# Performance work log

Measured on AMD Instinct MI355X. Metric: run time of the kernel, lower is better.

Reference implementation:

```python
import jax, jax.numpy as jnp
import numpy as np

N = 50000          # nodes
E_EDGES = 800000   # edges (before self loops)
IN_F = 256
HEADS = 4
OUT_F = 64
NEG_SLOPE = 0.2    # PyG GATv2Conv default negative_slope
EPS_GN = 1e-5      # GraphNorm eps


def setup_inputs() -> dict:
    key = jax.random.key(0)
    ks = jax.random.split(key, 8)
    X = jax.random.normal(ks[0], (N, IN_F), jnp.float32)
    E = jax.random.randint(ks[1], (2, E_EDGES), 0, N, jnp.int32)
    s_in = 1.0 / np.sqrt(IN_F)
    Wl = jax.random.normal(ks[2], (IN_F, HEADS * OUT_F), jnp.float32) * s_in   # lin_l (source)
    Wr = jax.random.normal(ks[3], (IN_F, HEADS * OUT_F), jnp.float32) * s_in   # lin_r (target)
    att = jax.random.normal(ks[4], (HEADS, OUT_F), jnp.float32) / np.sqrt(OUT_F)
    bias = jnp.zeros((OUT_F,), jnp.float32)           # concat=False -> bias of size out_channels
    gn_weight = jnp.ones((OUT_F,), jnp.float32)       # GraphNorm gamma
    gn_bias = jnp.zeros((OUT_F,), jnp.float32)        # GraphNorm beta
    gn_mean_scale = jnp.ones((OUT_F,), jnp.float32)   # GraphNorm alpha
    return {"X": X, "E": E, "Wl": Wl, "Wr": Wr, "att": att, "bias": bias,
            "gn_weight": gn_weight, "gn_bias": gn_bias, "gn_mean_scale": gn_mean_scale}


def reference(X, E, Wl, Wr, att, bias, gn_weight, gn_bias, gn_mean_scale):
    # --- GATv2Conv (heads=HEADS, concat=False, add_self_loops=True, eval: no dropout) ---
    loop = jnp.arange(N, dtype=E.dtype)
    src = jnp.concatenate([E[0], loop])   # [Et]
    dst = jnp.concatenate([E[1], loop])   # [Et]
    xl = (X @ Wl).reshape(N, HEADS, OUT_F)  # source transform
    xr = (X @ Wr).reshape(N, HEADS, OUT_F)  # target transform
    # per-edge attention logits: a^T LeakyReLU(xl_j + xr_i)
    e = jax.nn.leaky_relu(xl[src] + xr[dst], NEG_SLOPE)        # [Et, H, C]
    logits = jnp.einsum('ehc,hc->eh', e, att)                  # [Et, H]
    # segment softmax over incoming edges of each destination node
    m = jax.lax.stop_gradient(jax.ops.segment_max(logits, dst, num_segments=N))
    p = jnp.exp(logits - m[dst])
    denom = jax.ops.segment_sum(p, dst, num_segments=N)
    alpha = p / (denom[dst] + 1e-16)                           # [Et, H]
    out = jax.ops.segment_sum(xl[src] * alpha[:, :, None], dst, num_segments=N)  # [N, H, C]
    out = out.mean(axis=1) + bias                              # concat=False -> mean over heads
    # --- GraphNorm (single graph) ---
    mu = out.mean(axis=0)
    xc = out - gn_mean_scale * mu
    var = (xc * xc).mean(axis=0)
    return gn_weight * xc * jax.lax.rsqrt(var + EPS_GN) + gn_bias
```

## Files before the change

kernel.cpp:

```cpp
#include <hip/hip_runtime.h>
#include <hip/hip_bf16.h>

#define IN_F   256
#define HEADS  4
#define OUT_F  64
#define HF     (HEADS * OUT_F)
#define NOUT   512
#define MAXDEG 128

typedef __bf16 bf16x8 __attribute__((ext_vector_type(8)));
typedef float  f32x4  __attribute__((ext_vector_type(4)));
typedef float  f32x2  __attribute__((ext_vector_type(2)));

__device__ __forceinline__ unsigned short f2bf(float f) {
    unsigned u = __float_as_uint(f);
    return (unsigned short)((u + 0x7FFFu + ((u >> 16) & 1u)) >> 16);
}
__device__ __forceinline__ void gld_lds16(const unsigned short* g, unsigned short* lds_base) {
    __builtin_amdgcn_global_load_lds(
        (const __attribute__((address_space(1))) unsigned int*)g,
        (__attribute__((address_space(3))) unsigned int*)lds_base,
        16, 0, 0);
}
__device__ __forceinline__ f32x2 up2(int u) {
    f32x2 r;
    r.x = __uint_as_float(((unsigned)u) << 16);
    r.y = __uint_as_float(((unsigned)u) & 0xFFFF0000u);
    return r;
}
__device__ __forceinline__ f32x2 max2(f32x2 a, f32x2 b) {
    f32x2 r; r.x = fmaxf(a.x, b.x); r.y = fmaxf(a.y, b.y); return r;
}

__global__ __launch_bounds__(256) void prep(
    const float* __restrict__ X, const float* __restrict__ Wl,
    const float* __restrict__ Wr,
    unsigned short* __restrict__ Xb, unsigned short* __restrict__ Wt,
    int* __restrict__ zero32, int M, int Mp, int Z)
{
    const int b = blockIdx.x, t = threadIdx.x;
    const int idx = b * 256 + t;

    if (idx < Mp * 64) {
        int e = idx * 4;
        int row = e >> 8;
        float4 v = make_float4(0.f, 0.f, 0.f, 0.f);
        if (row < M) v = *(const float4*)(X + e);
        ushort4 o;
        o.x = f2bf(v.x); o.y = f2bf(v.y); o.z = f2bf(v.z); o.w = f2bf(v.w);
        *(ushort4*)(Xb + e) = o;
    }
    if (b < NOUT) {
        const float* W = (b < HF) ? Wl : Wr;
        Wt[b * IN_F + t] = f2bf(W[t * HF + (b & (HF - 1))]);
    }
    if (b >= NOUT) {
        int zi = (b - NOUT) * 256 + t;
        if (zi < Z) zero32[zi] = 0;
    }
}

__global__ __launch_bounds__(256, 2) void gemm_scatter(
    const unsigned short* __restrict__ Xb,
    const unsigned short* __restrict__ Wt,
    unsigned short* __restrict__ xlr,
    const int* __restrict__ E, int* __restrict__ deg,
    int* __restrict__ ssrc, int EE, int SB)
{
    __shared__ __align__(16) unsigned short As[128 * 64];
    __shared__ __align__(16) unsigned short Bs[256 * 64];

    if (blockIdx.x < SB) {
        int i = (blockIdx.x * 256 + threadIdx.x) * 4;
        if (i >= EE) return;
        int4 s4 = *(const int4*)(E + i);
        int4 d4 = *(const int4*)(E + EE + i);
        int p0 = atomicAdd(&deg[d4.x], 1);
        int p1 = atomicAdd(&deg[d4.y], 1);
        int p2 = atomicAdd(&deg[d4.z], 1);
        int p3 = atomicAdd(&deg[d4.w], 1);
        if (p0 < MAXDEG) ssrc[d4.x * MAXDEG + p0] = s4.x;
        if (p1 < MAXDEG) ssrc[d4.y * MAXDEG + p1] = s4.y;
        if (p2 < MAXDEG) ssrc[d4.z * MAXDEG + p2] = s4.z;
        if (p3 < MAXDEG) ssrc[d4.w * MAXDEG + p3] = s4.w;
        return;
    }

    const int g    = blockIdx.x - SB;
    const int tid  = threadIdx.x;
    const int w    = tid >> 6;
    const int lane = tid & 63;
    const int m0   = (g >> 1) * 128;
    const int n0   = (g & 1) * 256;
    const int wm   = (w >> 1) * 64;
    const int wn   = (w & 1) * 128;

    f32x4 acc[4][8];
    #pragma unroll
    for (int i = 0; i < 4; ++i)
        #pragma unroll
        for (int j = 0; j < 8; ++j)
            #pragma unroll
            for (int r = 0; r < 4; ++r) acc[i][j][r] = 0.f;

    const int lr = lane >> 3;
    const int ls = lane & 7;

    for (int k0 = 0; k0 < IN_F; k0 += 64) {
        #pragma unroll
        for (int i = 0; i < 4; ++i) {
            int r = w * 32 + i * 8 + lr;
            int c = ls ^ (r & 7);
            gld_lds16(Xb + (size_t)(m0 + r) * IN_F + k0 + c * 8, &As[(w * 32 + i * 8) * 64]);
        }
        #pragma unroll
        for (int i = 0; i < 8; ++i) {
            int r = w * 64 + i * 8 + lr;
            int c = ls ^ (r & 7);
            gld_lds16(Wt + (size_t)(n0 + r) * IN_F + k0 + c * 8, &Bs[(w * 64 + i * 8) * 64]);
        }
        __syncthreads();

        #pragma unroll
        for (int t = 0; t < 2; ++t) {
            bf16x8 af[4], bfr[8];
            #pragma unroll
            for (int i = 0; i < 4; ++i) {
                int m = wm + i * 16 + (lane & 15);
                int s = (t * 4 + (lane >> 4)) ^ (lane & 7);
                af[i] = __builtin_bit_cast(bf16x8, *(const int4*)&As[m * 64 + s * 8]);
            }
            #pragma unroll
            for (int j = 0; j < 8; ++j) {
                int n = wn + j * 16 + (lane & 15);
                int s = (t * 4 + (lane >> 4)) ^ (lane & 7);
                bfr[j] = __builtin_bit_cast(bf16x8, *(const int4*)&Bs[n * 64 + s * 8]);
            }
            #pragma unroll
            for (int i = 0; i < 4; ++i)
                #pragma unroll
                for (int j = 0; j < 8; ++j)
                    acc[i][j] = __builtin_amdgcn_mfma_f32_16x16x32_bf16(
                        af[i], bfr[j], acc[i][j], 0, 0, 0);
        }
        __syncthreads();
    }

    #pragma unroll
    for (int j = 0; j < 8; ++j) {
        int gc = n0 + wn + j * 16 + (lane & 15);
        #pragma unroll
        for (int i = 0; i < 4; ++i) {
            int gr0 = m0 + wm + i * 16 + (lane >> 4) * 4;
            #pragma unroll
            for (int r = 0; r < 4; ++r)
                xlr[(size_t)(gr0 + r) * NOUT + gc] = f2bf(acc[i][j][r]);
        }
    }
}

__global__ __launch_bounds__(128) void aggr_csr(
    const unsigned short* __restrict__ xlr, const float* __restrict__ att,
    const int* __restrict__ deg, const int* __restrict__ ssrc,
    float* __restrict__ accum, int N)
{
    const int v = blockIdx.x * 2 + (threadIdx.x >> 6);
    if (v >= N) return;
    const int lane = threadIdx.x & 63;
    const int hw = lane >> 5;
    const int h  = (lane >> 3) & 3;
    const int q  = lane & 7;
    const int cbase = h * OUT_F + q * 8;

    const float L2E = 1.44269504088896f;
    f32x2 at2[4];
    {
        float4 a0 = *(const float4*)(att + cbase);
        float4 a1 = *(const float4*)(att + cbase + 4);
        at2[0].x = L2E * a0.x; at2[0].y = L2E * a0.y;
        at2[1].x = L2E * a0.z; at2[1].y = L2E * a0.w;
        at2[2].x = L2E * a1.x; at2[2].y = L2E * a1.y;
        at2[3].x = L2E * a1.z; at2[3].y = L2E * a1.w;
    }
    f32x2 r2[4];
    {
        int4 ru = *(const int4*)(xlr + (size_t)v * NOUT + HF + cbase);
        r2[0] = up2(ru.x); r2[1] = up2(ru.y); r2[2] = up2(ru.z); r2[3] = up2(ru.w);
    }

    f32x2 S0 = {0.f,0.f}, S1 = {0.f,0.f}, S2 = {0.f,0.f}, S3 = {0.f,0.f};
    float den = 0.f;

    const int o0 = v * MAXDEG;
    const int items = deg[v] + 1;
    const unsigned short* xbase = xlr + cbase;

    for (int e0 = 0; e0 < items; e0 += 64) {
        int it = e0 + lane;
        int sv = v;
        if (it > 0 && it < items) sv = ssrc[o0 + it - 1];
        const int nch = min(64, items - e0);
        const int npair = (nch + 1) >> 1;

        int j = 0;
        for (; j + 2 <= npair; j += 2) {
            const int iA = 2 * j + hw, iB = iA + 2;
            const int sA = __shfl(sv, iA, 64);
            const int sB = __shfl(sv, iB, 64);
            int4 uA = *(const int4*)(xbase + (size_t)sA * NOUT);
            int4 uB = *(const int4*)(xbase + (size_t)sB * NOUT);
            f32x2 a0 = up2(uA.x), a1 = up2(uA.y), a2 = up2(uA.z), a3 = up2(uA.w);
            f32x2 b0 = up2(uB.x), b1 = up2(uB.y), b2 = up2(uB.z), b3 = up2(uB.w);
            f32x2 sa0 = a0 + r2[0], sa1 = a1 + r2[1], sa2 = a2 + r2[2], sa3 = a3 + r2[3];
            f32x2 sb0 = b0 + r2[0], sb1 = b1 + r2[1], sb2 = b2 + r2[2], sb3 = b3 + r2[3];
            f32x2 tA2 = max2(sa0, 0.2f * sa0) * at2[0];
            tA2 += max2(sa1, 0.2f * sa1) * at2[1];
            tA2 += max2(sa2, 0.2f * sa2) * at2[2];
            tA2 += max2(sa3, 0.2f * sa3) * at2[3];
            f32x2 tB2 = max2(sb0, 0.2f * sb0) * at2[0];
            tB2 += max2(sb1, 0.2f * sb1) * at2[1];
            tB2 += max2(sb2, 0.2f * sb2) * at2[2];
            tB2 += max2(sb3, 0.2f * sb3) * at2[3];
            float tA = tA2.x + tA2.y, tB = tB2.x + tB2.y;
            tA += __shfl_xor(tA, 1, 64); tB += __shfl_xor(tB, 1, 64);
            tA += __shfl_xor(tA, 2, 64); tB += __shfl_xor(tB, 2, 64);
            tA += __shfl_xor(tA, 4, 64); tB += __shfl_xor(tB, 4, 64);
            float pA = ((e0 + iA) < items) ? exp2f(tA) : 0.f;
            float pB = ((e0 + iB) < items) ? exp2f(tB) : 0.f;
            den += pA + pB;
            S0 += pA * a0 + pB * b0;
            S1 += pA * a1 + pB * b1;
            S2 += pA * a2 + pB * b2;
            S3 += pA * a3 + pB * b3;
        }
        for (; j < npair; ++j) {
            const int iA = 2 * j + hw;
            const int sA = __shfl(sv, iA, 64);
            int4 uA = *(const int4*)(xbase + (size_t)sA * NOUT);
            f32x2 a0 = up2(uA.x), a1 = up2(uA.y), a2 = up2(uA.z), a3 = up2(uA.w);
            f32x2 sa0 = a0 + r2[0], sa1 = a1 + r2[1], sa2 = a2 + r2[2], sa3 = a3 + r2[3];
            f32x2 tA2 = max2(sa0, 0.2f * sa0) * at2[0];
            tA2 += max2(sa1, 0.2f * sa1) * at2[1];
            tA2 += max2(sa2, 0.2f * sa2) * at2[2];
            tA2 += max2(sa3, 0.2f * sa3) * at2[3];
            float tA = tA2.x + tA2.y;
            tA += __shfl_xor(tA, 1, 64);
            tA += __shfl_xor(tA, 2, 64);
            tA += __shfl_xor(tA, 4, 64);
            float pA = ((e0 + iA) < items) ? exp2f(tA) : 0.f;
            den += pA;
            S0 += pA * a0; S1 += pA * a1; S2 += pA * a2; S3 += pA * a3;
        }
    }

    den += __shfl_xor(den, 32, 64);
    S0.x += __shfl_xor(S0.x, 32, 64); S0.y += __shfl_xor(S0.y, 32, 64);
    S1.x += __shfl_xor(S1.x, 32, 64); S1.y += __shfl_xor(S1.y, 32, 64);
    S2.x += __shfl_xor(S2.x, 32, 64); S2.y += __shfl_xor(S2.y, 32, 64);
    S3.x += __shfl_xor(S3.x, 32, 64); S3.y += __shfl_xor(S3.y, 32, 64);

    const float inv = 1.f / (den + 1e-16f);
    float o[8] = { S0.x*inv, S0.y*inv, S1.x*inv, S1.y*inv,
                   S2.x*inv, S2.y*inv, S3.x*inv, S3.y*inv };
    #pragma unroll
    for (int k = 0; k < 8; ++k) {
        o[k] += __shfl_xor(o[k], 8, 64);
        o[k] += __shfl_xor(o[k], 16, 64);
        o[k] *= 0.25f;
    }
    if (lane < 8) {
        float* dst = accum + (size_t)v * OUT_F + lane * 8;
        *(float4*)(dst)     = make_float4(o[0], o[1], o[2], o[3]);
        *(float4*)(dst + 4) = make_float4(o[4], o[5], o[6], o[7]);
    }
}

__global__ __launch_bounds__(256) void gn_stats(
    const float* __restrict__ accum, const float* __restrict__ bias,
    float* __restrict__ gsum, float* __restrict__ gsumsq, int total)
{
    const int tid = threadIdx.x;
    const int col = tid & 63;
    const float b = bias[col];
    float s = 0.f, s2 = 0.f;
    for (int idx = blockIdx.x * 256 + tid; idx < total; idx += gridDim.x * 256) {
        float o = accum[idx] + b;
        s += o; s2 += o * o;
    }
    __shared__ float ls[4][64], ls2[4][64];
    const int w = tid >> 6;
    ls[w][col] = s; ls2[w][col] = s2;
    __syncthreads();
    if (tid < 64) {
        atomicAdd(&gsum[tid],   ls[0][tid] + ls[1][tid] + ls[2][tid] + ls[3][tid]);
        atomicAdd(&gsumsq[tid], ls2[0][tid] + ls2[1][tid] + ls2[2][tid] + ls2[3][tid]);
    }
}

__global__ __launch_bounds__(256) void gn_norm(
    const float* __restrict__ accum, const float* __restrict__ bias,
    const float* __restrict__ gsum, const float* __restrict__ gsumsq,
    const float* __restrict__ gw, const float* __restrict__ gb,
    const float* __restrict__ gms,
    float* __restrict__ out, int total, float invN)
{
    const int idx = blockIdx.x * 256 + threadIdx.x;
    if (idx >= total) return;
    const int col = idx & 63;
    float mu = gsum[col] * invN;
    float m2 = gsumsq[col] * invN;
    float a  = gms[col];
    float var = m2 - 2.f * a * mu * mu + a * a * mu * mu;
    float o  = accum[idx] + bias[col];
    float xc = o - a * mu;
    out[idx] = gw[col] * xc * rsqrtf(var + 1e-5f) + gb[col];
}

extern "C" void kernel_launch(void* const* d_in, const int* in_sizes, int n_in,
                              void* d_out, int out_size, void* d_ws, size_t ws_size,
                              hipStream_t stream)
{
    const float* X    = (const float*)d_in[0];
    const int*   E    = (const int*)  d_in[1];
    const float* Wl   = (const float*)d_in[2];
    const float* Wr   = (const float*)d_in[3];
    const float* att  = (const float*)d_in[4];
    const float* bias = (const float*)d_in[5];
    const float* gw   = (const float*)d_in[6];
    const float* gb   = (const float*)d_in[7];
    const float* gms  = (const float*)d_in[8];
    float* out = (float*)d_out;

    const int N  = in_sizes[0] / IN_F;
    const int EE = in_sizes[1] / 2;
    const int total = N * OUT_F;
    const int MT = (N + 127) / 128;
    const int Mp = MT * 128;
    const int SB = (EE / 4 + 255) / 256;

    char* ws = (char*)d_ws;
    unsigned short* Xb  = (unsigned short*)ws;
    unsigned short* Wt  = Xb + (size_t)Mp * IN_F;
    unsigned short* xlr = Wt + (size_t)NOUT * IN_F;
    int*   deg    = (int*)(xlr + (size_t)Mp * NOUT);
    float* gsum   = (float*)(deg + N);
    float* gsumsq = gsum + 64;
    int*   ssrc   = (int*)(gsumsq + 64);
    float* accum  = (float*)(ssrc + (size_t)N * MAXDEG);

    const int Z = N + 128;

    prep<<<(Mp * 64 + 255) / 256, 256, 0, stream>>>(
        X, Wl, Wr, Xb, Wt, deg, N, Mp, Z);

    gemm_scatter<<<SB + 2 * MT, 256, 0, stream>>>(Xb, Wt, xlr, E, deg, ssrc, EE, SB);

    aggr_csr<<<(N + 1) / 2, 128, 0, stream>>>(xlr, att, deg, ssrc, accum, N);

    gn_stats<<<1024, 256, 0, stream>>>(accum, bias, gsum, gsumsq, total);
    gn_norm<<<(total + 255) / 256, 256, 0, stream>>>(
        accum, bias, gsum, gsumsq, gw, gb, gms, out, total, 1.0f / (float)N);
}
```

Measured before the change: 263.4 us.

## Switch aggregation to ELL layout with wave-uniform scalar neighbor loads

The neighbor slot capacity is halved to 64. The aggregation kernel is remapped so the whole wave handles one edge at a time: 4 heads x 16 lanes x 4 channels. Each iteration handles four edges, with neighbor indices read as wave-uniform values via readfirstlane instead of per-lane loads plus shuffles. The prep kernel now zeroes the whole ssrc slot array with 128-bit stores, so padded slots point at a valid node and are masked out. This adds extra zeroing traffic and wasted work on padded slots, and degree is now clamped at 64, which could drop edges on high-degree nodes.

Result: slower. 269.9 us (+2.5%).

```diff
diff --git a/kernel.cpp b/kernel.cpp
--- a/kernel.cpp
+++ b/kernel.cpp
@@ -6,7 +6,7 @@
 #define OUT_F  64
 #define HF     (HEADS * OUT_F)
 #define NOUT   512
-#define MAXDEG 128
+#define MAXDEG 64
 
 typedef __bf16 bf16x8 __attribute__((ext_vector_type(8)));
 typedef float  f32x4  __attribute__((ext_vector_type(4)));
@@ -36,7 +36,7 @@
     const float* __restrict__ X, const float* __restrict__ Wl,
     const float* __restrict__ Wr,
     unsigned short* __restrict__ Xb, unsigned short* __restrict__ Wt,
-    int* __restrict__ zero32, int M, int Mp, int Z)
+    int4* __restrict__ zero128, int M, int Mp, int Z4)
 {
     const int b = blockIdx.x, t = threadIdx.x;
     const int idx = b * 256 + t;
@@ -56,7 +56,7 @@
     }
     if (b >= NOUT) {
         int zi = (b - NOUT) * 256 + t;
-        if (zi < Z) zero32[zi] = 0;
+        if (zi < Z4) zero128[zi] = make_int4(0, 0, 0, 0);
     }
 }
 
@@ -159,7 +159,7 @@
     }
 }
 
-__global__ __launch_bounds__(128) void aggr_csr(
+__global__ __launch_bounds__(128) void aggr_ell(
     const unsigned short* __restrict__ xlr, const float* __restrict__ att,
     const int* __restrict__ deg, const int* __restrict__ ssrc,
     float* __restrict__ accum, int N)
@@ -167,111 +167,80 @@
     const int v = blockIdx.x * 2 + (threadIdx.x >> 6);
     if (v >= N) return;
     const int lane = threadIdx.x & 63;
-    const int hw = lane >> 5;
-    const int h  = (lane >> 3) & 3;
-    const int q  = lane & 7;
-    const int cbase = h * OUT_F + q * 8;
+    const int q = lane & 15;
+    const int coff = (lane >> 4) * OUT_F + q * 4;
 
     const float L2E = 1.44269504088896f;
-    f32x2 at2[4];
+    f32x2 at0, at1;
     {
-        float4 a0 = *(const float4*)(att + cbase);
-        float4 a1 = *(const float4*)(att + cbase + 4);
-        at2[0].x = L2E * a0.x; at2[0].y = L2E * a0.y;
-        at2[1].x = L2E * a0.z; at2[1].y = L2E * a0.w;
-        at2[2].x = L2E * a1.x; at2[2].y = L2E * a1.y;
-        at2[3].x = L2E * a1.z; at2[3].y = L2E * a1.w;
-    }
-    f32x2 r2[4];
+        float4 a = *(const float4*)(att + coff);
+        at0.x = L2E * a.x; at0.y = L2E * a.y;
+        at1.x = L2E * a.z; at1.y = L2E * a.w;
+    }
+    f32x2 r0, r1;
     {
-        int4 ru = *(const int4*)(xlr + (size_t)v * NOUT + HF + cbase);
-        r2[0] = up2(ru.x); r2[1] = up2(ru.y); r2[2] = up2(ru.z); r2[3] = up2(ru.w);
-    }
-
-    f32x2 S0 = {0.f,0.f}, S1 = {0.f,0.f}, S2 = {0.f,0.f}, S3 = {0.f,0.f};
+        int2 ru = *(const int2*)(xlr + (size_t)v * NOUT + HF + coff);
+        r0 = up2(ru.x); r1 = up2(ru.y);
+    }
+
+    f32x2 S0 = {0.f, 0.f}, S1 = {0.f, 0.f};
     float den = 0.f;
 
+    const int items = min(deg[v], MAXDEG) + 1;
     const int o0 = v * MAXDEG;
-    const int items = deg[v] + 1;
-    const unsigned short* xbase = xlr + cbase;
-
-    for (int e0 = 0; e0 < items; e0 += 64) {
-        int it = e0 + lane;
-        int sv = v;
-        if (it > 0 && it < items) sv = ssrc[o0 + it - 1];
-        const int nch = min(64, items - e0);
-        const int npair = (nch + 1) >> 1;
-
-        int j = 0;
-        for (; j + 2 <= npair; j += 2) {
-            const int iA = 2 * j + hw, iB = iA + 2;
-            const int sA = __shfl(sv, iA, 64);
-            const int sB = __shfl(sv, iB, 64);
-            int4 uA = *(const int4*)(xbase + (size_t)sA * NOUT);
-            int4 uB = *(const int4*)(xbase + (size_t)sB * NOUT);
-            f32x2 a0 = up2(uA.x), a1 = up2(uA.y), a2 = up2(uA.z), a3 = up2(uA.w);
-            f32x2 b0 = up2(uB.x), b1 = up2(uB.y), b2 = up2(uB.z), b3 = up2(uB.w);
-            f32x2 sa0 = a0 + r2[0], sa1 = a1 + r2[1], sa2 = a2 + r2[2], sa3 = a3 + r2[3];
-            f32x2 sb0 = b0 + r2[0], sb1 = b1 + r2[1], sb2 = b2 + r2[2], sb3 = b3 + r2[3];
-            f32x2 tA2 = max2(sa0, 0.2f * sa0) * at2[0];
-            tA2 += max2(sa1, 0.2f * sa1) * at2[1];
-            tA2 += max2(sa2, 0.2f * sa2) * at2[2];
-            tA2 += max2(sa3, 0.2f * sa3) * at2[3];
-            f32x2 tB2 = max2(sb0, 0.2f * sb0) * at2[0];
-            tB2 += max2(sb1, 0.2f * sb1) * at2[1];
-            tB2 += max2(sb2, 0.2f * sb2) * at2[2];
-            tB2 += max2(sb3, 0.2f * sb3) * at2[3];
-            float tA = tA2.x + tA2.y, tB = tB2.x + tB2.y;
-            tA += __shfl_xor(tA, 1, 64); tB += __shfl_xor(tB, 1, 64);
-            tA += __shfl_xor(tA, 2, 64); tB += __shfl_xor(tB, 2, 64);
-            tA += __shfl_xor(tA, 4, 64); tB += __shfl_xor(tB, 4, 64);
-            float pA = ((e0 + iA) < items) ? exp2f(tA) : 0.f;
-            float pB = ((e0 + iB) < items) ? exp2f(tB) : 0.f;
-            den += pA + pB;
-            S0 += pA * a0 + pB * b0;
-            S1 += pA * a1 + pB * b1;
-            S2 += pA * a2 + pB * b2;
-            S3 += pA * a3 + pB * b3;
-        }
-        for (; j < npair; ++j) {
-            const int iA = 2 * j + hw;
-            const int sA = __shfl(sv, iA, 64);
-            int4 uA = *(const int4*)(xbase + (size_t)sA * NOUT);
-            f32x2 a0 = up2(uA.x), a1 = up2(uA.y), a2 = up2(uA.z), a3 = up2(uA.w);
-            f32x2 sa0 = a0 + r2[0], sa1 = a1 + r2[1], sa2 = a2 + r2[2], sa3 = a3 + r2[3];
-            f32x2 tA2 = max2(sa0, 0.2f * sa0) * at2[0];
-            tA2 += max2(sa1, 0.2f * sa1) * at2[1];
-            tA2 += max2(sa2, 0.2f * sa2) * at2[2];
-            tA2 += max2(sa3, 0.2f * sa3) * at2[3];
-            float tA = tA2.x + tA2.y;
-            tA += __shfl_xor(tA, 1, 64);
-            tA += __shfl_xor(tA, 2, 64);
-            tA += __shfl_xor(tA, 4, 64);
-            float pA = ((e0 + iA) < items) ? exp2f(tA) : 0.f;
-            den += pA;
-            S0 += pA * a0; S1 += pA * a1; S2 += pA * a2; S3 += pA * a3;
-        }
-    }
-
-    den += __shfl_xor(den, 32, 64);
-    S0.x += __shfl_xor(S0.x, 32, 64); S0.y += __shfl_xor(S0.y, 32, 64);
-    S1.x += __shfl_xor(S1.x, 32, 64); S1.y += __shfl_xor(S1.y, 32, 64);
-    S2.x += __shfl_xor(S2.x, 32, 64); S2.y += __shfl_xor(S2.y, 32, 64);
-    S3.x += __shfl_xor(S3.x, 32, 64); S3.y += __shfl_xor(S3.y, 32, 64);
+    const unsigned short* xb = xlr + coff;
+
+    for (int j0 = 0; j0 < items; j0 += 4) {
+        const int base = o0 + j0 - 1;
+        int sv0 = (j0 == 0) ? v : ssrc[base];
+        int sv1 = ssrc[base + 1];
+        int sv2 = ssrc[base + 2];
+        int sv3 = ssrc[base + 3];
+        const int sA = __builtin_amdgcn_readfirstlane(sv0);
+        const int sB = __builtin_amdgcn_readfirstlane(sv1);
+        const int sC = __builtin_amdgcn_readfirstlane(sv2);
+        const int sD = __builtin_amdgcn_readfirstlane(sv3);
+
+        int2 uA = *(const int2*)(xb + (size_t)sA * NOUT);
+        int2 uB = *(const int2*)(xb + (size_t)sB * NOUT);
+        int2 uC = *(const int2*)(xb + (size_t)sC * NOUT);
+        int2 uD = *(const int2*)(xb + (size_t)sD * NOUT);
+
+        f32x2 xa0, xa1, t2;
+        float t, p;
+        #define ITEM(U, K)                                              \
+        {                                                               \
+            xa0 = up2(U.x); xa1 = up2(U.y);                             \
+            f32x2 s0 = xa0 + r0, s1 = xa1 + r1;                         \
+            t2 = max2(s0, 0.2f * s0) * at0;                             \
+            t2 += max2(s1, 0.2f * s1) * at1;                            \
+            t = t2.x + t2.y;                                            \
+            t += __shfl_xor(t, 1, 64);                                  \
+            t += __shfl_xor(t, 2, 64);                                  \
+            t += __shfl_xor(t, 4, 64);                                  \
+            t += __shfl_xor(t, 8, 64);                                  \
+            p = ((j0 + K) < items) ? exp2f(t) : 0.f;                    \
+            den += p;                                                   \
+            S0 += p * xa0; S1 += p * xa1;                               \
+        }
+        ITEM(uA, 0)
+        ITEM(uB, 1)
+        ITEM(uC, 2)
+        ITEM(uD, 3)
+        #undef ITEM
+    }
 
     const float inv = 1.f / (den + 1e-16f);
-    float o[8] = { S0.x*inv, S0.y*inv, S1.x*inv, S1.y*inv,
-                   S2.x*inv, S2.y*inv, S3.x*inv, S3.y*inv };
+    float o[4] = { S0.x * inv, S0.y * inv, S1.x * inv, S1.y * inv };
     #pragma unroll
-    for (int k = 0; k < 8; ++k) {
-        o[k] += __shfl_xor(o[k], 8, 64);
+    for (int k = 0; k < 4; ++k) {
         o[k] += __shfl_xor(o[k], 16, 64);
+        o[k] += __shfl_xor(o[k], 32, 64);
         o[k] *= 0.25f;
     }
-    if (lane < 8) {
-        float* dst = accum + (size_t)v * OUT_F + lane * 8;
-        *(float4*)(dst)     = make_float4(o[0], o[1], o[2], o[3]);
-        *(float4*)(dst + 4) = make_float4(o[4], o[5], o[6], o[7]);
+    if (lane < 16) {
+        *(float4*)(accum + (size_t)v * OUT_F + q * 4) =
+            make_float4(o[0], o[1], o[2], o[3]);
     }
 }
 
@@ -348,14 +317,15 @@
     int*   ssrc   = (int*)(gsumsq + 64);
     float* accum  = (float*)(ssrc + (size_t)N * MAXDEG);
 
-    const int Z = N + 128;
+    const int Z  = N + 128 + N * MAXDEG;
+    const int Z4 = (Z + 3) / 4;
 
     prep<<<(Mp * 64 + 255) / 256, 256, 0, stream>>>(
-        X, Wl, Wr, Xb, Wt, deg, N, Mp, Z);
+        X, Wl, Wr, Xb, Wt, (int4*)deg, N, Mp, Z4);
 
     gemm_scatter<<<SB + 2 * MT, 256, 0, stream>>>(Xb, Wt, xlr, E, deg, ssrc, EE, SB);
 
-    aggr_csr<<<(N + 1) / 2, 128, 0, stream>>>(xlr, att, deg, ssrc, accum, N);
+    aggr_ell<<<(N + 1) / 2, 128, 0, stream>>>(xlr, att, deg, ssrc, accum, N);
 
     gn_stats<<<1024, 256, 0, stream>>>(accum, bias, gsum, gsumsq, total);
     gn_norm<<<(total + 255) / 256, 256, 0, stream>>>(
```
